# Kernel optimization log

Measured on AMD Instinct MI355X. Metric: run time of the kernel, lower is better.

## Reference

```python
import jax, jax.numpy as jnp
import numpy as np

N, E = 50000, 1_000_000
CH = [128, 64, 64]  # channels list -> 2 GATv2 layers
NEG_SLOPE = 0.2


def setup_inputs() -> dict:
    key = jax.random.key(0)
    ks = jax.random.split(key, 16)
    inp = {
        "x": jax.random.normal(ks[0], (N, CH[0]), jnp.float32),
        "edge_index": jax.random.randint(ks[1], (2, E), 0, N, jnp.int32),
        "edge_attr": jax.random.uniform(ks[2], (E, 1), jnp.float32),
    }
    i = 3
    for l in range(2):
        cin, cout = CH[l], CH[l + 1]
        g = (2.0 / (cin + cout)) ** 0.5  # glorot-ish scale
        inp[f"Wl{l}"] = jax.random.normal(ks[i], (cin, cout), jnp.float32) * g; i += 1
        inp[f"bl{l}"] = jnp.zeros((cout,), jnp.float32)
        inp[f"Wr{l}"] = jax.random.normal(ks[i], (cin, cout), jnp.float32) * g; i += 1
        inp[f"br{l}"] = jnp.zeros((cout,), jnp.float32)
        inp[f"We{l}"] = jax.random.normal(ks[i], (1, cout), jnp.float32) * g; i += 1
        inp[f"att{l}"] = jax.random.normal(ks[i], (cout,), jnp.float32) * (1.0 / cout ** 0.5); i += 1
        inp[f"bias{l}"] = jnp.zeros((cout,), jnp.float32)
    return inp


def _gatv2_layer(h, src, dst, ea, Wl, bl, Wr, br, We, att, bias):
    # PyG GATv2Conv, heads=1, concat=False, share_weights=False
    n = h.shape[0]
    xj = (h @ Wl + bl)[src]          # lin_l(x) gathered at source  [Et, C]
    xi = (h @ Wr + br)[dst]          # lin_r(x) gathered at target  [Et, C]
    e = ea @ We                      # lin_edge(edge_attr)          [Et, C]
    z = jax.nn.leaky_relu(xi + xj + e, NEG_SLOPE)
    logits = z @ att                 # [Et]
    # numerically-stable segment softmax over target node
    m = jax.ops.segment_max(logits, dst, num_segments=n)
    ex = jnp.exp(logits - m[dst])
    s = jax.ops.segment_sum(ex, dst, num_segments=n)
    alpha = ex / s[dst]              # [Et]
    out = jax.ops.segment_sum(xj * alpha[:, None], dst, num_segments=n)
    return out + bias


def reference(x, edge_index, edge_attr,
              Wl0, bl0, Wr0, br0, We0, att0, bias0,
              Wl1, bl1, Wr1, br1, We1, att1, bias1):
    n = x.shape[0]
    # add self loops with fill_value=1 for edge_attr (PyG default add_self_loops=True)
    loop = jnp.arange(n, dtype=edge_index.dtype)
    src = jnp.concatenate([edge_index[0], loop])
    dst = jnp.concatenate([edge_index[1], loop])
    ea = jnp.concatenate([edge_attr, jnp.ones((n, 1), edge_attr.dtype)], axis=0)
    h = _gatv2_layer(x, src, dst, ea, Wl0, bl0, Wr0, br0, We0, att0, bias0)
    h = _gatv2_layer(h, src, dst, ea, Wl1, bl1, Wr1, br1, We1, att1, bias1)
    return h
```

## Files before the change

### kernel.cpp

```cpp
#include <hip/hip_runtime.h>
#include <math.h>

#define NPB_SHIFT 7
#define NPB 128
#define NBK_MAX 512
#define BCAP 3584

typedef _Float16 f16x2 __attribute__((ext_vector_type(2)));
union F16U { f16x2 v; unsigned int u; };


__global__ __launch_bounds__(1024) void k_scatter_agg(
    const int* __restrict__ src, const int* __restrict__ dst,
    const float* __restrict__ ea, int E, int nbk, int chunk,
    int* bcur, int2* __restrict__ tmp) {
  __shared__ int lcnt[NBK_MAX], lcnt2[NBK_MAX], lbase[NBK_MAX];
  int t = threadIdx.x;
  for (int i = t; i < nbk; i += 1024) { lcnt[i] = 0; lcnt2[i] = 0; }
  __syncthreads();
  int c0 = blockIdx.x * chunk;
  int c1 = min(E, c0 + chunk);
  for (int e = c0 + t; e < c1; e += 1024)
    atomicAdd(&lcnt[dst[e] >> NPB_SHIFT], 1);
  __syncthreads();
  for (int i = t; i < nbk; i += 1024) {
    int c = lcnt[i];
    lbase[i] = c ? (i * BCAP + atomicAdd(&bcur[i], c)) : 0;
  }
  __syncthreads();
  for (int e = c0 + t; e < c1; e += 1024) {
    int d = dst[e];
    int b = d >> NPB_SHIFT;
    int pos = lbase[b] + atomicAdd(&lcnt2[b], 1);
    tmp[pos] = make_int2(((d & (NPB - 1)) << 20) | src[e], __float_as_int(ea[e]));
  }
}

__global__ __launch_bounds__(256) void k_bucket_to_csr(
    const int2* __restrict__ tmp, const int* __restrict__ bcur,
    int N, int ET, int2* __restrict__ eidx, int* __restrict__ row_ptr) {
  __shared__ int cnt[NPB], sc[NPB], cur[NPB];
  __shared__ int wsum[4];
  int b = blockIdx.x;
  int n0 = b << NPB_SHIFT;
  int nn = min(NPB, N - n0);
  int t = threadIdx.x;
  int psum = 0;
  for (int i = t; i < b; i += 256) psum += bcur[i];
  #pragma unroll
  for (int off = 32; off; off >>= 1) psum += __shfl_xor(psum, off, 64);
  if ((t & 63) == 0) wsum[t >> 6] = psum;
  if (t < NPB) cnt[t] = 0;
  __syncthreads();
  int prefix = wsum[0] + wsum[1] + wsum[2] + wsum[3];
  int cb = bcur[b];
  int i0 = b * BCAP, i1 = i0 + cb;
  for (int i = i0 + t; i < i1; i += 256)
    atomicAdd(&cnt[(tmp[i].x >> 20) & (NPB - 1)], 1);
  __syncthreads();
  int v = (t < NPB) ? cnt[t] : 0;
  int x = v;
  if (t < NPB) sc[t] = x;
  __syncthreads();
  for (int off = 1; off < NPB; off <<= 1) {
    int y = (t >= off && t < NPB) ? sc[t - off] : 0;
    __syncthreads();
    if (t < NPB) { x += y; sc[t] = x; }
    __syncthreads();
  }
  int w0 = prefix + n0;
  if (t < nn) {
    int node = n0 + t;
    int base = w0 + (x - v) + t;
    row_ptr[node] = base;
    eidx[base] = make_int2(node, __float_as_int(1.0f));
    cur[t] = base + 1;
  }
  if (b == 0 && t == 0) row_ptr[N] = ET;
  __syncthreads();
  for (int i = i0 + t; i < i1; i += 256) {
    int2 r = tmp[i];
    int pos = atomicAdd(&cur[(r.x >> 20) & (NPB - 1)], 1);
    eidx[pos] = make_int2(r.x & 0xFFFFF, r.y);
  }
}


template<int CIN>
__global__ __launch_bounds__(256) void k_lin2_tiled(
    const float* __restrict__ h,
    const float* __restrict__ Wl, const float* __restrict__ bl,
    const float* __restrict__ Wr, const float* __restrict__ br,
    _Float16* __restrict__ xlh, _Float16* __restrict__ xrh, int N) {
  __shared__ float sW[64][128];
  __shared__ float sH[64][64];
  const int t = threadIdx.x;
  const int row0 = blockIdx.x * 64;
  const int c4 = (t & 31) * 4;
  const int rr = (t >> 5) * 8;

  float acc[8][4];
  #pragma unroll
  for (int r = 0; r < 8; r++)
    #pragma unroll
    for (int c = 0; c < 4; c++) acc[r][c] = 0.f;

  for (int kt = 0; kt < CIN; kt += 64) {
    __syncthreads();
    #pragma unroll
    for (int i = 0; i < 8; i++) {
      int flat = i * 1024 + t * 4;
      int k = flat >> 7, j = flat & 127;
      const float* Wsrc = (j < 64) ? Wl : Wr;
      *(float4*)&sW[k][j] = *(const float4*)&Wsrc[(size_t)(kt + k) * 64 + (j & 63)];
    }
    #pragma unroll
    for (int i = 0; i < 4; i++) {
      int flat = i * 1024 + t * 4;
      int r = flat >> 6, k = flat & 63;
      float4 v = make_float4(0.f, 0.f, 0.f, 0.f);
      if (row0 + r < N) v = *(const float4*)&h[(size_t)(row0 + r) * CIN + kt + k];
      *(float4*)&sH[r][k] = v;
    }
    __syncthreads();
    #pragma unroll 8
    for (int k = 0; k < 64; k++) {
      float4 w = *(float4*)&sW[k][c4];
      #pragma unroll
      for (int r = 0; r < 8; r++) {
        float hv = sH[rr + r][k];
        acc[r][0] = fmaf(hv, w.x, acc[r][0]);
        acc[r][1] = fmaf(hv, w.y, acc[r][1]);
        acc[r][2] = fmaf(hv, w.z, acc[r][2]);
        acc[r][3] = fmaf(hv, w.w, acc[r][3]);
      }
    }
  }

  const float* bsrc = (c4 < 64) ? bl : br;
  float bv[4];
  #pragma unroll
  for (int c = 0; c < 4; c++) bv[c] = bsrc[(c4 & 63) + c];
  _Float16* o = (c4 < 64) ? xlh : xrh;
  #pragma unroll
  for (int r = 0; r < 8; r++) {
    int row = row0 + rr + r;
    if (row < N) {
      F16U ua, ub;
      ua.v = (f16x2){(_Float16)(acc[r][0] + bv[0]), (_Float16)(acc[r][1] + bv[1])};
      ub.v = (f16x2){(_Float16)(acc[r][2] + bv[2]), (_Float16)(acc[r][3] + bv[3])};
      *(uint2*)&o[(size_t)row * 64 + (c4 & 63)] = make_uint2(ua.u, ub.u);
    }
  }
}


#define RESCALE_THR 8.0f

__global__ __launch_bounds__(256) void k_gat_edge(
    const _Float16* __restrict__ xlh, const _Float16* __restrict__ xrh,
    const int* __restrict__ row_ptr, const int2* __restrict__ eidx,
    const float* __restrict__ We, const float* __restrict__ att,
    const float* __restrict__ bias,
    float* __restrict__ out, int N) {
  int n = (blockIdx.x * blockDim.x + threadIdx.x) >> 6;
  if (n >= N) return;
  int lane = threadIdx.x & 63;
  int g = lane >> 4;
  int cb = (lane & 15) * 4;

  uint2 xiu = *(const uint2*)&xrh[(size_t)n * 64 + cb];
  F16U uxa, uxb; uxa.u = xiu.x; uxb.u = xiu.y;
  f16x2 xi01 = uxa.v, xi23 = uxb.v;
  float4 wef = *(const float4*)&We[cb];
  float4 atf = *(const float4*)&att[cb];
  f16x2 we01 = {(_Float16)wef.x, (_Float16)wef.y};
  f16x2 we23 = {(_Float16)wef.z, (_Float16)wef.w};
  f16x2 at01 = {(_Float16)atf.x, (_Float16)atf.y};
  f16x2 at23 = {(_Float16)atf.z, (_Float16)atf.w};
  const f16x2 zz  = {(_Float16)0.f, (_Float16)0.f};
  const f16x2 c02 = {(_Float16)0.2f, (_Float16)0.2f};

  int e0 = row_ptr[n], e1 = row_ptr[n + 1];

  float m = -INFINITY, s = 0.f;
  float4 acc = make_float4(0.f, 0.f, 0.f, 0.f);

  int e = e0 + g;
  int2 metaA = make_int2(0, 0), metaB = make_int2(0, 0);
  uint2 rawA = make_uint2(0, 0), rawB = make_uint2(0, 0);
  if (e < e1) {
    metaA = eidx[e];
    rawA = *(const uint2*)&xlh[(size_t)metaA.x * 64 + cb];
  }
  if (e + 4 < e1) {
    metaB = eidx[e + 4];
    rawB = *(const uint2*)&xlh[(size_t)metaB.x * 64 + cb];
  }

  while (e < e1) {
    int2 cm = metaA;
    uint2 craw = rawA;
    metaA = metaB;
    rawA = rawB;
    int en2 = e + 8;
    if (en2 < e1) {
      metaB = eidx[en2];
      rawB = *(const uint2*)&xlh[(size_t)metaB.x * 64 + cb];
    }
    F16U u0, u1; u0.u = craw.x; u1.u = craw.y;
    f16x2 xj01 = u0.v, xj23 = u1.v;
    float eav = __int_as_float(cm.y);
    _Float16 eah = (_Float16)eav;
    f16x2 ea2 = {eah, eah};
    f16x2 z01 = __builtin_elementwise_fma(ea2, we01, xi01 + xj01);
    f16x2 z23 = __builtin_elementwise_fma(ea2, we23, xi23 + xj23);
    f16x2 l01 = __builtin_elementwise_fma(
        c02, __builtin_elementwise_min(z01, zz), __builtin_elementwise_max(z01, zz));
    f16x2 l23 = __builtin_elementwise_fma(
        c02, __builtin_elementwise_min(z23, zz), __builtin_elementwise_max(z23, zz));
    float p = __builtin_amdgcn_fdot2(l01, at01,
              __builtin_amdgcn_fdot2(l23, at23, 0.f, false), false);
    #pragma unroll
    for (int off = 1; off < 16; off <<= 1) p += __shfl_xor(p, off, 64);
    if (p > m + RESCALE_THR) {
      float coef = __expf(m - p);
      s = fmaf(s, coef, 1.f);
      acc.x = fmaf(acc.x, coef, (float)xj01[0]);
      acc.y = fmaf(acc.y, coef, (float)xj01[1]);
      acc.z = fmaf(acc.z, coef, (float)xj23[0]);
      acc.w = fmaf(acc.w, coef, (float)xj23[1]);
      m = p;
    } else {
      float wgt = __expf(p - m);
      s += wgt;
      acc.x = fmaf(wgt, (float)xj01[0], acc.x);
      acc.y = fmaf(wgt, (float)xj01[1], acc.y);
      acc.z = fmaf(wgt, (float)xj23[0], acc.z);
      acc.w = fmaf(wgt, (float)xj23[1], acc.w);
    }
    e += 4;
  }

  #pragma unroll
  for (int off = 16; off <= 32; off <<= 1) {
    float mo = __shfl_xor(m, off, 64);
    float so = __shfl_xor(s, off, 64);
    float4 ao;
    ao.x = __shfl_xor(acc.x, off, 64);
    ao.y = __shfl_xor(acc.y, off, 64);
    ao.z = __shfl_xor(acc.z, off, 64);
    ao.w = __shfl_xor(acc.w, off, 64);
    float mn = fmaxf(m, mo);
    float cs = (m == -INFINITY) ? 0.f : __expf(m - mn);
    float co = (mo == -INFINITY) ? 0.f : __expf(mo - mn);
    s = s * cs + so * co;
    acc.x = acc.x * cs + ao.x * co;
    acc.y = acc.y * cs + ao.y * co;
    acc.z = acc.z * cs + ao.z * co;
    acc.w = acc.w * cs + ao.w * co;
    m = mn;
  }

  if (g == 0) {
    float inv = 1.0f / s;
    float4 o;
    o.x = acc.x * inv + bias[cb + 0];
    o.y = acc.y * inv + bias[cb + 1];
    o.z = acc.z * inv + bias[cb + 2];
    o.w = acc.w * inv + bias[cb + 3];
    *(float4*)&out[(size_t)n * 64 + cb] = o;
  }
}


extern "C" void kernel_launch(void* const* d_in, const int* in_sizes, int n_in,
                              void* d_out, int out_size, void* d_ws, size_t ws_size,
                              hipStream_t stream) {
  const float* x    = (const float*)d_in[0];
  const int*   ei   = (const int*)d_in[1];
  const float* ea   = (const float*)d_in[2];
  const float* Wl0  = (const float*)d_in[3];
  const float* bl0  = (const float*)d_in[4];
  const float* Wr0  = (const float*)d_in[5];
  const float* br0  = (const float*)d_in[6];
  const float* We0  = (const float*)d_in[7];
  const float* att0 = (const float*)d_in[8];
  const float* bias0= (const float*)d_in[9];
  const float* Wl1  = (const float*)d_in[10];
  const float* bl1  = (const float*)d_in[11];
  const float* Wr1  = (const float*)d_in[12];
  const float* br1  = (const float*)d_in[13];
  const float* We1  = (const float*)d_in[14];
  const float* att1 = (const float*)d_in[15];
  const float* bias1= (const float*)d_in[16];

  const int N  = in_sizes[0] / 128;
  const int E  = in_sizes[1] / 2;
  const int ET = E + N;
  const int* src = ei;
  const int* dst = ei + E;
  const int nbk = (N + NPB - 1) >> NPB_SHIFT;

  char* w = (char*)d_ws;
  _Float16* xlh  = (_Float16*)w; w += (size_t)N * 64 * 2;
  _Float16* xrh  = (_Float16*)w; w += (size_t)N * 64 * 2;
  float*  h1     = (float*)w;  w += (size_t)N * 64 * 4;
  int*    row_ptr= (int*)w;    w += (size_t)(N + 2) * 4;
  int2*   eidx   = (int2*)w;   w += (size_t)ET * 8;
  int*    bcur   = (int*)w;    w += NBK_MAX * 4;
  int2*   tmp    = (int2*)xlh;

  float* out = (float*)d_out;

  {
    int nblk = 256;
    int chunk = (E + nblk - 1) / nblk;
    hipMemsetAsync(bcur, 0, (size_t)nbk * 4, stream);
    k_scatter_agg<<<nblk, 1024, 0, stream>>>(src, dst, ea, E, nbk, chunk, bcur, tmp);
    k_bucket_to_csr<<<nbk, 256, 0, stream>>>(tmp, bcur, N, ET, eidx, row_ptr);
  }

  {
    int nblk = (N + 63) / 64;
    k_lin2_tiled<128><<<nblk, 256, 0, stream>>>(x, Wl0, bl0, Wr0, br0, xlh, xrh, N);
    k_gat_edge<<<(N + 3) / 4, 256, 0, stream>>>(xlh, xrh, row_ptr, eidx, We0, att0, bias0, h1, N);
  }
  {
    int nblk = (N + 63) / 64;
    k_lin2_tiled<64><<<nblk, 256, 0, stream>>>(h1, Wl1, bl1, Wr1, br1, xlh, xrh, N);
    k_gat_edge<<<(N + 3) / 4, 256, 0, stream>>>(xlh, xrh, row_ptr, eidx, We1, att1, bias1, out, N);
  }
}
```

Baseline: 180.0 us.

## Use MFMA f16 matmul for node projections and store layer-1 output as half

Replaces the scalar FP32 tiled projection kernel with an MFMA 16x16x16 f16 kernel. Weights are transposed into padded shared memory as half, and inputs are converted to half on load. The intermediate layer-1 activations are now written as f16, which halves that tensor's write and read traffic and lets the second projection load half input directly. This trades FP32 matmul precision for f16 inputs, and the output stores are now scalar per-element rather than vectorised.

```diff
diff --git a/kernel.cpp b/kernel.cpp
--- a/kernel.cpp
+++ b/kernel.cpp
@@ -7,6 +7,8 @@
 #define BCAP 3584
 
 typedef _Float16 f16x2 __attribute__((ext_vector_type(2)));
+typedef _Float16 f16x4 __attribute__((ext_vector_type(4)));
+typedef float f32x4 __attribute__((ext_vector_type(4)));
 union F16U { f16x2 v; unsigned int u; };
 
 
@@ -86,83 +88,104 @@
 }
 
 
-template<int CIN>
-__global__ __launch_bounds__(256) void k_lin2_tiled(
-    const float* __restrict__ h,
+template<int CIN, bool IN_HALF>
+__global__ __launch_bounds__(256) void k_lin2_mfma(
+    const void* __restrict__ hin,
     const float* __restrict__ Wl, const float* __restrict__ bl,
     const float* __restrict__ Wr, const float* __restrict__ br,
     _Float16* __restrict__ xlh, _Float16* __restrict__ xrh, int N) {
-  __shared__ float sW[64][128];
-  __shared__ float sH[64][64];
+  constexpr int LDK = CIN + 8;
+  __shared__ _Float16 sA[64 * LDK];
+  __shared__ _Float16 sBt[128 * LDK];
   const int t = threadIdx.x;
   const int row0 = blockIdx.x * 64;
-  const int c4 = (t & 31) * 4;
-  const int rr = (t >> 5) * 8;
-
-  float acc[8][4];
-  #pragma unroll
-  for (int r = 0; r < 8; r++)
+
+  {
+    int c = t >> 1, half = t & 1;
+    const float* Wsrc = (c < 64) ? Wl : Wr;
+    int col = c & 63;
+    int k0 = half * (CIN / 2);
+    #pragma unroll 4
+    for (int k = 0; k < CIN / 2; k += 2) {
+      float w0 = Wsrc[(size_t)(k0 + k) * 64 + col];
+      float w1 = Wsrc[(size_t)(k0 + k + 1) * 64 + col];
+      F16U u; u.v = (f16x2){(_Float16)w0, (_Float16)w1};
+      *(unsigned int*)&sBt[c * LDK + k0 + k] = u.u;
+    }
+  }
+  #pragma unroll
+  for (int i = 0; i < CIN / 16; i++) {
+    int flat = i * 1024 + t * 4;
+    int r = flat / CIN, k = flat & (CIN - 1);
+    uint2 w;
+    if constexpr (IN_HALF) {
+      const _Float16* h = (const _Float16*)hin;
+      w = (row0 + r < N) ? *(const uint2*)&h[(size_t)(row0 + r) * CIN + k]
+                         : make_uint2(0, 0);
+    } else {
+      const float* h = (const float*)hin;
+      float4 v = make_float4(0.f, 0.f, 0.f, 0.f);
+      if (row0 + r < N) v = *(const float4*)&h[(size_t)(row0 + r) * CIN + k];
+      F16U ua, ub;
+      ua.v = (f16x2){(_Float16)v.x, (_Float16)v.y};
+      ub.v = (f16x2){(_Float16)v.z, (_Float16)v.w};
+      w = make_uint2(ua.u, ub.u);
+    }
+    *(uint2*)&sA[r * LDK + k] = w;
+  }
+  __syncthreads();
+
+  const int wid = t >> 6, lane = t & 63;
+  const int arow = (wid << 4) + (lane & 15);
+  const int koff = (lane >> 4) << 2;
+
+  float bv[8];
+  #pragma unroll
+  for (int ct = 0; ct < 8; ct++) {
+    int c = ct * 16 + (lane & 15);
+    bv[ct] = (c < 64) ? bl[c] : br[c & 63];
+  }
+
+  f32x4 acc[8];
+  #pragma unroll
+  for (int ct = 0; ct < 8; ct++) acc[ct] = (f32x4){0.f, 0.f, 0.f, 0.f};
+
+  const _Float16* aBase = &sA[arow * LDK + koff];
+  #pragma unroll
+  for (int ks = 0; ks < CIN; ks += 16) {
+    f16x4 a = *(const f16x4*)(aBase + ks);
     #pragma unroll
-    for (int c = 0; c < 4; c++) acc[r][c] = 0.f;
-
-  for (int kt = 0; kt < CIN; kt += 64) {
-    __syncthreads();
-    #pragma unroll
-    for (int i = 0; i < 8; i++) {
-      int flat = i * 1024 + t * 4;
-      int k = flat >> 7, j = flat & 127;
-      const float* Wsrc = (j < 64) ? Wl : Wr;
-      *(float4*)&sW[k][j] = *(const float4*)&Wsrc[(size_t)(kt + k) * 64 + (j & 63)];
-    }
-    #pragma unroll
-    for (int i = 0; i < 4; i++) {
-      int flat = i * 1024 + t * 4;
-      int r = flat >> 6, k = flat & 63;
-      float4 v = make_float4(0.f, 0.f, 0.f, 0.f);
-      if (row0 + r < N) v = *(const float4*)&h[(size_t)(row0 + r) * CIN + kt + k];
-      *(float4*)&sH[r][k] = v;
-    }
-    __syncthreads();
-    #pragma unroll 8
-    for (int k = 0; k < 64; k++) {
-      float4 w = *(float4*)&sW[k][c4];
+    for (int ct = 0; ct < 8; ct++) {
+      f16x4 b = *(const f16x4*)&sBt[(ct * 16 + (lane & 15)) * LDK + koff + ks];
+      acc[ct] = __builtin_amdgcn_mfma_f32_16x16x16f16(a, b, acc[ct], 0, 0, 0);
+    }
+  }
+
+  const int rbase = row0 + (wid << 4) + ((lane >> 4) << 2);
+  #pragma unroll
+  for (int j = 0; j < 4; j++) {
+    int row = rbase + j;
+    if (row < N) {
       #pragma unroll
-      for (int r = 0; r < 8; r++) {
-        float hv = sH[rr + r][k];
-        acc[r][0] = fmaf(hv, w.x, acc[r][0]);
-        acc[r][1] = fmaf(hv, w.y, acc[r][1]);
-        acc[r][2] = fmaf(hv, w.z, acc[r][2]);
-        acc[r][3] = fmaf(hv, w.w, acc[r][3]);
+      for (int ct = 0; ct < 8; ct++) {
+        int c = ct * 16 + (lane & 15);
+        _Float16* o = (c < 64) ? xlh : xrh;
+        o[(size_t)row * 64 + (c & 63)] = (_Float16)(acc[ct][j] + bv[ct]);
       }
     }
   }
-
-  const float* bsrc = (c4 < 64) ? bl : br;
-  float bv[4];
-  #pragma unroll
-  for (int c = 0; c < 4; c++) bv[c] = bsrc[(c4 & 63) + c];
-  _Float16* o = (c4 < 64) ? xlh : xrh;
-  #pragma unroll
-  for (int r = 0; r < 8; r++) {
-    int row = row0 + rr + r;
-    if (row < N) {
-      F16U ua, ub;
-      ua.v = (f16x2){(_Float16)(acc[r][0] + bv[0]), (_Float16)(acc[r][1] + bv[1])};
-      ub.v = (f16x2){(_Float16)(acc[r][2] + bv[2]), (_Float16)(acc[r][3] + bv[3])};
-      *(uint2*)&o[(size_t)row * 64 + (c4 & 63)] = make_uint2(ua.u, ub.u);
-    }
-  }
 }
 
 
 #define RESCALE_THR 8.0f
 
+template<bool OUT_HALF>
 __global__ __launch_bounds__(256) void k_gat_edge(
     const _Float16* __restrict__ xlh, const _Float16* __restrict__ xrh,
     const int* __restrict__ row_ptr, const int2* __restrict__ eidx,
     const float* __restrict__ We, const float* __restrict__ att,
     const float* __restrict__ bias,
-    float* __restrict__ out, int N) {
+    void* __restrict__ outp, int N) {
   int n = (blockIdx.x * blockDim.x + threadIdx.x) >> 6;
   if (n >= N) return;
   int lane = threadIdx.x & 63;
@@ -264,12 +287,18 @@
 
   if (g == 0) {
     float inv = 1.0f / s;
-    float4 o;
-    o.x = acc.x * inv + bias[cb + 0];
-    o.y = acc.y * inv + bias[cb + 1];
-    o.z = acc.z * inv + bias[cb + 2];
-    o.w = acc.w * inv + bias[cb + 3];
-    *(float4*)&out[(size_t)n * 64 + cb] = o;
+    float o0 = acc.x * inv + bias[cb + 0];
+    float o1 = acc.y * inv + bias[cb + 1];
+    float o2 = acc.z * inv + bias[cb + 2];
+    float o3 = acc.w * inv + bias[cb + 3];
+    if constexpr (OUT_HALF) {
+      F16U ua, ub;
+      ua.v = (f16x2){(_Float16)o0, (_Float16)o1};
+      ub.v = (f16x2){(_Float16)o2, (_Float16)o3};
+      *(uint2*)&((_Float16*)outp)[(size_t)n * 64 + cb] = make_uint2(ua.u, ub.u);
+    } else {
+      *(float4*)&((float*)outp)[(size_t)n * 64 + cb] = make_float4(o0, o1, o2, o3);
+    }
   }
 }
 
@@ -305,7 +334,7 @@
   char* w = (char*)d_ws;
   _Float16* xlh  = (_Float16*)w; w += (size_t)N * 64 * 2;
   _Float16* xrh  = (_Float16*)w; w += (size_t)N * 64 * 2;
-  float*  h1     = (float*)w;  w += (size_t)N * 64 * 4;
+  _Float16* h1h  = (_Float16*)w; w += (size_t)N * 64 * 2;
   int*    row_ptr= (int*)w;    w += (size_t)(N + 2) * 4;
   int2*   eidx   = (int2*)w;   w += (size_t)ET * 8;
   int*    bcur   = (int*)w;    w += NBK_MAX * 4;
@@ -316,19 +345,14 @@
   {
     int nblk = 256;
     int chunk = (E + nblk - 1) / nblk;
-    hipMemsetAsync(bcur, 0, (size_t)nbk * 4, stream);
+    (void)hipMemsetAsync(bcur, 0, (size_t)nbk * 4, stream);
     k_scatter_agg<<<nblk, 1024, 0, stream>>>(src, dst, ea, E, nbk, chunk, bcur, tmp);
     k_bucket_to_csr<<<nbk, 256, 0, stream>>>(tmp, bcur, N, ET, eidx, row_ptr);
   }
 
-  {
-    int nblk = (N + 63) / 64;
-    k_lin2_tiled<128><<<nblk, 256, 0, stream>>>(x, Wl0, bl0, Wr0, br0, xlh, xrh, N);
-    k_gat_edge<<<(N + 3) / 4, 256, 0, stream>>>(xlh, xrh, row_ptr, eidx, We0, att0, bias0, h1, N);
-  }
-  {
-    int nblk = (N + 63) / 64;
-    k_lin2_tiled<64><<<nblk, 256, 0, stream>>>(h1, Wl1, bl1, Wr1, br1, xlh, xrh, N);
-    k_gat_edge<<<(N + 3) / 4, 256, 0, stream>>>(xlh, xrh, row_ptr, eidx, We1, att1, bias1, out, N);
-  }
-}
+  int nblk = (N + 63) / 64;
+  k_lin2_mfma<128, false><<<nblk, 256, 0, stream>>>(x, Wl0, bl0, Wr0, br0, xlh, xrh, N);
+  k_gat_edge<true><<<(N + 3) / 4, 256, 0, stream>>>(xlh, xrh, row_ptr, eidx, We0, att0, bias0, h1h, N);
+  k_lin2_mfma<64, true><<<nblk, 256, 0, stream>>>(h1h, Wl1, bl1, Wr1, br1, xlh, xrh, N);
+  k_gat_edge<false><<<(N + 3) / 4, 256, 0, stream>>>(xlh, xrh, row_ptr, eidx, We1, att1, bias1, out, N);
+}
```

Result: faster. 157.0 us (median of 2 runs) (-12.8%).
